# Optimization experiments

Measured on AMD Instinct MI355X. Metric: run time of the kernel, lower is better.

Reference implementation:

```python
import jax, jax.numpy as jnp
import numpy as np

V, B, T, C, H, L = 32000, 4, 1024, 1024, 16, 8
HS = C // H  # head_size = 64


def _ln(x, g, b):
    m = x.mean(-1, keepdims=True)
    v = x.var(-1, keepdims=True)
    return (x - m) / jnp.sqrt(v + 1e-5) * g + b


def setup_inputs() -> dict:
    key = jax.random.key(0)
    ks = jax.random.split(key, 24)
    s = 0.02
    inp = {
        "idx": jax.random.randint(ks[0], (B, T), 0, V, dtype=jnp.int64),
        "tok_emb": jax.random.normal(ks[1], (V, C), jnp.float32) * s,
        "pos_emb": jax.random.normal(ks[2], (T, C), jnp.float32) * s,
        "Wq": jax.random.normal(ks[3], (L, H, C, HS), jnp.float32) * s,
        "Wk": jax.random.normal(ks[4], (L, H, C, HS), jnp.float32) * s,
        "Wv": jax.random.normal(ks[5], (L, H, C, HS), jnp.float32) * s,
        "Ph_w": jax.random.normal(ks[6], (L, H, HS, C), jnp.float32) * s,
        "Ph_b": jnp.zeros((L, H, C), jnp.float32),
        "Pm_w": jax.random.normal(ks[7], (L, C, C), jnp.float32) * s,
        "Pm_b": jnp.zeros((L, C), jnp.float32),
        "ln1_g": jnp.ones((L, C), jnp.float32),
        "ln1_b": jnp.zeros((L, C), jnp.float32),
        "ln2_g": jnp.ones((L, C), jnp.float32),
        "ln2_b": jnp.zeros((L, C), jnp.float32),
        "W1": jax.random.normal(ks[8], (L, C, 4 * C), jnp.float32) * s,
        "b1": jnp.zeros((L, 4 * C), jnp.float32),
        "W2": jax.random.normal(ks[9], (L, 4 * C, C), jnp.float32) * s,
        "b2": jnp.zeros((L, C), jnp.float32),
        "lnf_g": jnp.ones((C,), jnp.float32),
        "lnf_b": jnp.zeros((C,), jnp.float32),
        "head_w": jax.random.normal(ks[10], (C, V), jnp.float32) * s,
        "head_b": jnp.zeros((V,), jnp.float32),
    }
    return inp


def reference(idx, tok_emb, pos_emb, Wq, Wk, Wv, Ph_w, Ph_b, Pm_w, Pm_b,
              ln1_g, ln1_b, ln2_g, ln2_b, W1, b1, W2, b2, lnf_g, lnf_b,
              head_w, head_b):
    Bx, Tx = idx.shape
    x = tok_emb[idx] + pos_emb[:Tx]  # [B,T,C]
    mask = jnp.tril(jnp.ones((Tx, Tx), bool))
    scale = x.shape[-1] ** -0.5  # NOTE: original scales by n_embd**-0.5, not head_size
    n_layers = Wq.shape[0]
    for l in range(n_layers):
        xn = _ln(x, ln1_g[l], ln1_b[l])
        q = jnp.einsum('btc,hcs->bhts', xn, Wq[l])
        k = jnp.einsum('btc,hcs->bhts', xn, Wk[l])
        v = jnp.einsum('btc,hcs->bhts', xn, Wv[l])
        wei = jnp.einsum('bhts,bhus->bhtu', q, k) * scale
        wei = jnp.where(mask, wei, -jnp.inf)
        wei = jax.nn.softmax(wei, axis=-1)
        o = jnp.einsum('bhtu,bhus->bhts', wei, v)  # [B,H,T,HS]
        per = jnp.einsum('bhts,hsc->bhtc', o, Ph_w[l]) + Ph_b[l][None, :, None, :]
        sa = per.sum(axis=1) @ Pm_w[l] + Pm_b[l]  # combine heads, final proj
        x = x + sa
        xn2 = _ln(x, ln2_g[l], ln2_b[l])
        h = jax.nn.gelu(xn2 @ W1[l] + b1[l], approximate=False)
        x = x + h @ W2[l] + b2[l]
    x = _ln(x, lnf_g, lnf_b)
    return x @ head_w + head_b  # logits [B,T,V]
```

## Files before the change

### kernel.cpp

```cpp
#include <hip/hip_runtime.h>
#include <hip/hip_bf16.h>
#include <math.h>

static constexpr int V = 32000, B = 4, T = 1024, C = 1024, H = 16, NL = 8, HS = 64;
static constexpr int M = B * T;

typedef __bf16 bf16x8 __attribute__((ext_vector_type(8)));
typedef __bf16 bf16x4 __attribute__((ext_vector_type(4)));
typedef float f32x4 __attribute__((ext_vector_type(4)));

#define AS1 __attribute__((address_space(1)))
#define AS3 __attribute__((address_space(3)))

__global__ void k_embed(const int* __restrict__ idx, const float* __restrict__ tok,
                        const float* __restrict__ pos, float* __restrict__ x) {
  int g = blockIdx.x * blockDim.x + threadIdx.x;
  if (g >= M * C / 4) return;
  int c4 = g & 255;
  int bt = g >> 8;
  int t = bt & (T - 1);
  int row = idx[bt];
  float4 tv = *(const float4*)(tok + (size_t)row * C + c4 * 4);
  float4 pv = *(const float4*)(pos + (size_t)t * C + c4 * 4);
  float4 o;
  o.x = tv.x + pv.x; o.y = tv.y + pv.y; o.z = tv.z + pv.z; o.w = tv.w + pv.w;
  *(float4*)(x + (size_t)bt * C + c4 * 4) = o;
}

__global__ __launch_bounds__(256) void k_ln_bf(const float* __restrict__ x, const float* __restrict__ g,
                                               const float* __restrict__ b, __hip_bfloat16* __restrict__ y) {
  int row = blockIdx.x, tid = threadIdx.x;
  float4 v = ((const float4*)(x + (size_t)row * C))[tid];
  float s = v.x + v.y + v.z + v.w;
  float ss = v.x * v.x + v.y * v.y + v.z * v.z + v.w * v.w;
  for (int off = 32; off > 0; off >>= 1) {
    s += __shfl_down(s, off);
    ss += __shfl_down(ss, off);
  }
  __shared__ float sb[4], qb[4];
  int wid = tid >> 6;
  if ((tid & 63) == 0) { sb[wid] = s; qb[wid] = ss; }
  __syncthreads();
  float st = sb[0] + sb[1] + sb[2] + sb[3];
  float qt = qb[0] + qb[1] + qb[2] + qb[3];
  float mean = st * (1.0f / C);
  float var = qt * (1.0f / C) - mean * mean;
  float rstd = rsqrtf(var + 1e-5f);
  float4 gv = ((const float4*)g)[tid];
  float4 bv = ((const float4*)b)[tid];
  union { __hip_bfloat16 h[4]; ushort4 u; } pk;
  pk.h[0] = __float2bfloat16((v.x - mean) * rstd * gv.x + bv.x);
  pk.h[1] = __float2bfloat16((v.y - mean) * rstd * gv.y + bv.y);
  pk.h[2] = __float2bfloat16((v.z - mean) * rstd * gv.z + bv.z);
  pk.h[3] = __float2bfloat16((v.w - mean) * rstd * gv.w + bv.w);
  *(ushort4*)(y + (size_t)row * C + tid * 4) = pk.u;
}

__device__ __forceinline__ void transp_block(const float* __restrict__ in, __hip_bfloat16* __restrict__ out,
                                             int K, int N, int bx, int by, float (*t)[65]) {
  int n0 = bx * 64, k0 = by * 64;
  int tx = threadIdx.x & 15, ty = threadIdx.x >> 4;
#pragma unroll
  for (int i = 0; i < 64; i += 16) {
    float4 v = *(const float4*)(in + (size_t)(k0 + ty + i) * N + n0 + tx * 4);
    t[ty + i][tx * 4 + 0] = v.x;
    t[ty + i][tx * 4 + 1] = v.y;
    t[ty + i][tx * 4 + 2] = v.z;
    t[ty + i][tx * 4 + 3] = v.w;
  }
  __syncthreads();
#pragma unroll
  for (int i = 0; i < 64; i += 16) {
    int n = ty + i;
    union { __hip_bfloat16 h[4]; ushort4 u; } pk;
#pragma unroll
    for (int j = 0; j < 4; ++j) pk.h[j] = __float2bfloat16(t[tx * 4 + j][n]);
    *(ushort4*)(out + (size_t)(n0 + n) * K + k0 + tx * 4) = pk.u;
  }
}

__global__ __launch_bounds__(256) void k_transp(const float* __restrict__ in, __hip_bfloat16* __restrict__ out,
                                                int K, int N) {
  __shared__ float t[64][65];
  transp_block(in, out, K, N, blockIdx.x, blockIdx.y, t);
}

__global__ __launch_bounds__(256) void k_prep(const float* __restrict__ Wq, const float* __restrict__ Wk,
                                              const float* __restrict__ Wv, const float* __restrict__ Pm,
                                              const float* __restrict__ Ph, const float* __restrict__ W1,
                                              const float* __restrict__ W2,
                                              __hip_bfloat16* __restrict__ qkvw, __hip_bfloat16* __restrict__ pmT,
                                              __hip_bfloat16* __restrict__ phB, __hip_bfloat16* __restrict__ w1T,
                                              __hip_bfloat16* __restrict__ w2T) {
  __shared__ float tls[64][65];
  int bid = blockIdx.x;
  if (bid < 768) {
    int bx = bid & 15, z = bid >> 4;
    int sel = z >> 4, h = z & 15;
    const float* W = sel == 0 ? Wq : (sel == 1 ? Wk : Wv);
    const float* in = W + (size_t)h * C * HS;
    __hip_bfloat16* o = qkvw + ((size_t)sel * 1024 + h * 64) * C;
    int k0 = bx * 64;
    int tx = threadIdx.x & 15, ty = threadIdx.x >> 4;
#pragma unroll
    for (int i = 0; i < 64; i += 16) {
      float4 v = *(const float4*)(in + (size_t)(k0 + ty + i) * HS + tx * 4);
      tls[ty + i][tx * 4 + 0] = v.x;
      tls[ty + i][tx * 4 + 1] = v.y;
      tls[ty + i][tx * 4 + 2] = v.z;
      tls[ty + i][tx * 4 + 3] = v.w;
    }
    __syncthreads();
#pragma unroll
    for (int i = 0; i < 64; i += 16) {
      int n = ty + i;
      union { __hip_bfloat16 h4[4]; ushort4 u; } pk;
#pragma unroll
      for (int j = 0; j < 4; ++j) pk.h4[j] = __float2bfloat16(tls[tx * 4 + j][n]);
      *(ushort4*)(o + (size_t)n * C + k0 + tx * 4) = pk.u;
    }
  } else if (bid < 1024) {
    int r = bid - 768;
    transp_block(Pm, pmT, C, C, r & 15, r >> 4, tls);
  } else if (bid < 2048) {
    int g = (bid - 1024) * 256 + threadIdx.x;
    float4 v = ((const float4*)Ph)[g];
    union { __hip_bfloat16 h[4]; ushort4 u; } pk;
    pk.h[0] = __float2bfloat16(v.x);
    pk.h[1] = __float2bfloat16(v.y);
    pk.h[2] = __float2bfloat16(v.z);
    pk.h[3] = __float2bfloat16(v.w);
    ((ushort4*)phB)[g] = pk.u;
  } else if (bid < 3072) {
    int r = bid - 2048;
    transp_block(W1, w1T, C, 4 * C, r & 63, r >> 6, tls);
  } else {
    int r = bid - 3072;
    transp_block(W2, w2T, 4 * C, C, r & 15, r >> 4, tls);
  }
}

__global__ __launch_bounds__(256) void k_biasc(const float* __restrict__ phb, const float* __restrict__ Pm,
                                               const float* __restrict__ Pmb, float* __restrict__ bc) {
  __shared__ float bs[1024];
  __shared__ float red[4][64];
  int tid = threadIdx.x;
#pragma unroll
  for (int q = 0; q < 4; ++q) {
    int c = tid * 4 + q;
    float s = 0.0f;
    for (int h = 0; h < H; ++h) s += phb[(size_t)h * C + c];
    bs[c] = s;
  }
  __syncthreads();
  int c = blockIdx.x * 64 + (tid & 63);
  int part = tid >> 6;
  float s = 0.0f;
  for (int j = part * 256; j < part * 256 + 256; ++j) s += bs[j] * Pm[(size_t)j * C + c];
  red[part][tid & 63] = s;
  __syncthreads();
  if (tid < 64)
    bc[blockIdx.x * 64 + tid] = Pmb[blockIdx.x * 64 + tid] + red[0][tid] + red[1][tid] + red[2][tid] + red[3][tid];
}

template <int BIAS, int GELU, int RES, int OUTBF>
__global__ __launch_bounds__(256) void k_gemm_bf(const __hip_bfloat16* __restrict__ A,
                                                 const __hip_bfloat16* __restrict__ Bt,
                                                 void* Cout, const float* __restrict__ bias,
                                                 const float* res, int N, int K) {
  __shared__ __align__(16) __hip_bfloat16 As[128 * 32];
  __shared__ __align__(16) __hip_bfloat16 Bs[128 * 32];
  int bm = blockIdx.y * 128, bn = blockIdx.x * 128;
  int tid = threadIdx.x;
  int w = tid >> 6, l = tid & 63;
  int wr = (w >> 1) * 64, wc = (w & 1) * 64;
  int lr = l >> 2;
  int lk = (l & 3) * 8;
  int fr = l & 15;
  int fk = (l >> 4) * 8;
  const __hip_bfloat16* Ag = A + (size_t)bm * K;
  const __hip_bfloat16* Bg = Bt + (size_t)bn * K;
  f32x4 acc[4][4];
#pragma unroll
  for (int m = 0; m < 4; ++m)
#pragma unroll
    for (int n = 0; n < 4; ++n) acc[m][n] = (f32x4){0.f, 0.f, 0.f, 0.f};

  for (int k0 = 0; k0 < K; k0 += 32) {
    __syncthreads();
#pragma unroll
    for (int i = 0; i < 2; ++i) {
      int seg = w * 2 + i;
      int r = seg * 16 + lr;
      __builtin_amdgcn_global_load_lds((const AS1 void*)(Ag + (size_t)r * K + k0 + lk),
                                       (AS3 void*)(As + seg * 512), 16, 0, 0);
      __builtin_amdgcn_global_load_lds((const AS1 void*)(Bg + (size_t)r * K + k0 + lk),
                                       (AS3 void*)(Bs + seg * 512), 16, 0, 0);
    }
    __syncthreads();
    bf16x8 af[4], bfr[4];
#pragma unroll
    for (int m = 0; m < 4; ++m) af[m] = *(const bf16x8*)(As + ((size_t)(wr + m * 16 + fr)) * 32 + fk);
#pragma unroll
    for (int n = 0; n < 4; ++n) bfr[n] = *(const bf16x8*)(Bs + ((size_t)(wc + n * 16 + fr)) * 32 + fk);
#pragma unroll
    for (int m = 0; m < 4; ++m)
#pragma unroll
      for (int n = 0; n < 4; ++n)
        acc[m][n] = __builtin_amdgcn_mfma_f32_16x16x32_bf16(af[m], bfr[n], acc[m][n], 0, 0, 0);
  }
  int crow0 = (l >> 4) * 4;
  int ccol = l & 15;
#pragma unroll
  for (int m = 0; m < 4; ++m) {
    int row = bm + wr + m * 16 + crow0;
#pragma unroll
    for (int n = 0; n < 4; ++n) {
      int col = bn + wc + n * 16 + ccol;
      float bv = BIAS ? bias[col] : 0.0f;
#pragma unroll
      for (int r = 0; r < 4; ++r) {
        float v = acc[m][n][r] + bv;
        if (GELU) v = 0.5f * v * (1.0f + erff(v * 0.70710678118f));
        if (RES) v += res[(size_t)(row + r) * N + col];
        if (OUTBF)
          ((__hip_bfloat16*)Cout)[(size_t)(row + r) * N + col] = __float2bfloat16(v);
        else
          ((float*)Cout)[(size_t)(row + r) * N + col] = v;
      }
    }
  }
}

template <int BIAS, int GELU, int RES, int OUTBF>
__global__ __launch_bounds__(512, 2) void k_gemm256(const __hip_bfloat16* __restrict__ Ah,
                                                    const __hip_bfloat16* __restrict__ Bth,
                                                    void* Cout, const float* __restrict__ bias,
                                                    const float* res, int N, int K) {
  __shared__ __align__(16) __bf16 As[4][256 * 32];
  __shared__ __align__(16) __bf16 Bs[4][256 * 32];
  const __bf16* A = (const __bf16*)Ah;
  const __bf16* Bt = (const __bf16*)Bth;
  const int nx = N >> 8;
  const int bid = blockIdx.x;
  const int sw = ((bid & 7) * ((int)gridDim.x >> 3)) + (bid >> 3);
  const int bn = (sw % nx) << 8;
  const int bm = (sw / nx) << 8;
  const int tid = threadIdx.x, w = tid >> 6, l = tid & 63;
  const int wm = w >> 2, wn = w & 3;
  const int fr = l & 15, fg = l >> 4;
  const int srow = w * 32 + (l >> 2);
  const int scole = ((((l & 3) << 4) ^ ((l & 8) << 2) ^ (l & 16)) >> 1);
  const __bf16* Ag = A + (size_t)(bm + srow) * K + scole;
  const __bf16* Bg = Bt + (size_t)(bn + srow) * K + scole;
  const int arow = wm * 128 + fr;
  const int brow = wn * 64 + fr;
  const int koff = (((fg * 16) ^ (((fr & 2) << 4) | ((fr & 4) << 2))) >> 1);

  f32x4 acc[8][4];
#pragma unroll
  for (int m = 0; m < 8; ++m)
#pragma unroll
    for (int n = 0; n < 4; ++n) acc[m][n] = (f32x4){0.f, 0.f, 0.f, 0.f};

  auto stage = [&](int bufi, int tt) {
    size_t kb = (size_t)tt * 32;
#pragma unroll
    for (int jj = 0; jj < 2; ++jj) {
      __builtin_amdgcn_global_load_lds((const AS1 void*)(Ag + (size_t)jj * 16 * K + kb),
                                       (AS3 void*)(&As[bufi][(w * 32 + jj * 16) * 32]), 16, 0, 0);
      __builtin_amdgcn_global_load_lds((const AS1 void*)(Bg + (size_t)jj * 16 * K + kb),
                                       (AS3 void*)(&Bs[bufi][(w * 32 + jj * 16) * 32]), 16, 0, 0);
    }
  };

  bf16x8 fa[2][8], fb[2][4];

#define READF(SET, BI)                                                              \
  {                                                                                 \
    const int bi_ = (BI);                                                           \
    _Pragma("unroll") for (int mg = 0; mg < 8; ++mg)                                \
        fa[SET][mg] = *(const bf16x8*)(&As[bi_][(arow + mg * 16) * 32 + koff]);     \
    _Pragma("unroll") for (int ng = 0; ng < 4; ++ng)                                \
        fb[SET][ng] = *(const bf16x8*)(&Bs[bi_][(brow + ng * 16) * 32 + koff]);     \
  }

#define MFMAS(SET)                                                                  \
  _Pragma("unroll") for (int mg = 0; mg < 8; ++mg)                                  \
      _Pragma("unroll") for (int ng = 0; ng < 4; ++ng)                              \
          acc[mg][ng] =                                                             \
              __builtin_amdgcn_mfma_f32_16x16x32_bf16(fa[SET][mg], fb[SET][ng], acc[mg][ng], 0, 0, 0);

#define GITER(T, CUR, NXT)                                                          \
  {                                                                                 \
    const int t_ = (T);                                                             \
    asm volatile("s_waitcnt lgkmcnt(0)" ::: "memory");                              \
    if (t_ + 2 < NT)                                                                \
      asm volatile("s_waitcnt vmcnt(4)" ::: "memory");                              \
    else                                                                            \
      asm volatile("s_waitcnt vmcnt(0)" ::: "memory");                              \
    __builtin_amdgcn_sched_barrier(0);                                              \
    __builtin_amdgcn_s_barrier();                                                   \
    __builtin_amdgcn_sched_barrier(0);                                              \
    if (t_ + 1 < NT) READF(NXT, (t_ + 1) & 3);                                      \
    if (t_ + 3 < NT) stage((t_ + 3) & 3, t_ + 3);                                   \
    __builtin_amdgcn_s_setprio(1);                                                  \
    MFMAS(CUR);                                                                     \
    __builtin_amdgcn_s_setprio(0);                                                  \
  }

  const int NT = K >> 5;
  stage(0, 0);
  stage(1, 1);
  stage(2, 2);
  asm volatile("s_waitcnt vmcnt(8)" ::: "memory");
  __builtin_amdgcn_sched_barrier(0);
  __builtin_amdgcn_s_barrier();
  __builtin_amdgcn_sched_barrier(0);
  READF(0, 0);

  for (int t = 0; t < NT; t += 2) {
    GITER(t, 0, 1);
    GITER(t + 1, 1, 0);
  }
#undef READF
#undef MFMAS
#undef GITER

#pragma unroll
  for (int mg = 0; mg < 8; ++mg) {
    int row = bm + wm * 128 + mg * 16 + fg * 4;
#pragma unroll
    for (int n = 0; n < 4; ++n) {
      int col = bn + wn * 64 + n * 16 + fr;
      float bvx = BIAS ? bias[col] : 0.0f;
#pragma unroll
      for (int r = 0; r < 4; ++r) {
        float v = acc[mg][n][r] + bvx;
        if (GELU) v = 0.5f * v * (1.0f + erff(v * 0.70710678118f));
        if (RES) v += res[(size_t)(row + r) * N + col];
        if (OUTBF)
          ((__hip_bfloat16*)Cout)[(size_t)(row + r) * N + col] = __float2bfloat16(v);
        else
          ((float*)Cout)[(size_t)(row + r) * N + col] = v;
      }
    }
  }
}

__global__ __launch_bounds__(256) void k_attn(const __hip_bfloat16* __restrict__ qkvh,
                                              __hip_bfloat16* __restrict__ o) {
  const __bf16* qkv = (const __bf16*)qkvh;
  int qi = blockIdx.x;
  int bh = blockIdx.y;
  int b = bh >> 4, h = bh & 15;
  int tid = threadIdx.x;
  int w = tid >> 6, l = tid & 63;
  int fr = l & 15, fg = l >> 4;
  int qw = qi * 64 + w * 16;

  __shared__ __align__(16) __bf16 Ks[32][72];
  __shared__ __align__(16) __bf16 Vt[64][40];
  __shared__ __align__(16) __bf16 Ps[4][16][40];

  const size_t bT = (size_t)b * T;
  bf16x8 a_q[2];
  {
    const __bf16* qp = qkv + (bT + qw + fr) * 3072 + h * 64 + fg * 8;
    a_q[0] = *(const bf16x8*)qp;
    a_q[1] = *(const bf16x8*)(qp + 32);
  }
  f32x4 acc_o[4];
#pragma unroll
  for (int n = 0; n < 4; ++n) acc_o[n] = (f32x4){0.f, 0.f, 0.f, 0.f};
  float mrow[4] = {-1e30f, -1e30f, -1e30f, -1e30f};
  float lrow[4] = {0.f, 0.f, 0.f, 0.f};

  int sr = tid >> 3;
  int sc = (tid & 7) * 8;
  int ntile = (qi + 1) * 2;
  for (int t = 0; t < ntile; ++t) {
    int kv0 = t * 32;
    __syncthreads();
    {
      const __bf16* kp = qkv + (bT + kv0 + sr) * 3072 + 1024 + h * 64 + sc;
      bf16x8 k8 = *(const bf16x8*)kp;
      bf16x8 v8 = *(const bf16x8*)(kp + 1024);
      *(bf16x8*)&Ks[sr][sc] = k8;
#pragma unroll
      for (int j = 0; j < 8; ++j) Vt[sc + j][sr] = v8[j];
    }
    __syncthreads();
    if (kv0 > qw + 15) continue;

    f32x4 s0 = (f32x4){0.f, 0.f, 0.f, 0.f}, s1 = s0;
    s0 = __builtin_amdgcn_mfma_f32_16x16x32_bf16(a_q[0], *(const bf16x8*)&Ks[fr][fg * 8], s0, 0, 0, 0);
    s0 = __builtin_amdgcn_mfma_f32_16x16x32_bf16(a_q[1], *(const bf16x8*)&Ks[fr][32 + fg * 8], s0, 0, 0, 0);
    s1 = __builtin_amdgcn_mfma_f32_16x16x32_bf16(a_q[0], *(const bf16x8*)&Ks[16 + fr][fg * 8], s1, 0, 0, 0);
    s1 = __builtin_amdgcn_mfma_f32_16x16x32_bf16(a_q[1], *(const bf16x8*)&Ks[16 + fr][32 + fg * 8], s1, 0, 0, 0);

    int qrow = qw + fg * 4;
#pragma unroll
    for (int r = 0; r < 4; ++r) { s0[r] *= 0.03125f; s1[r] *= 0.03125f; }
    if (kv0 + 31 > qw) {
#pragma unroll
      for (int r = 0; r < 4; ++r) {
        if (kv0 + fr > qrow + r) s0[r] = -1e30f;
        if (kv0 + 16 + fr > qrow + r) s1[r] = -1e30f;
      }
    }
    float tm[4], psum[4], alpha[4];
#pragma unroll
    for (int r = 0; r < 4; ++r) tm[r] = fmaxf(s0[r], s1[r]);
#pragma unroll
    for (int off = 1; off < 16; off <<= 1)
#pragma unroll
      for (int r = 0; r < 4; ++r) tm[r] = fmaxf(tm[r], __shfl_xor(tm[r], off));
#pragma unroll
    for (int r = 0; r < 4; ++r) {
      float mnew = fmaxf(mrow[r], tm[r]);
      alpha[r] = __expf(mrow[r] - mnew);
      mrow[r] = mnew;
      float p0 = __expf(s0[r] - mnew);
      float p1 = __expf(s1[r] - mnew);
      s0[r] = p0; s1[r] = p1;
      psum[r] = p0 + p1;
    }
#pragma unroll
    for (int off = 1; off < 16; off <<= 1)
#pragma unroll
      for (int r = 0; r < 4; ++r) psum[r] += __shfl_xor(psum[r], off);
#pragma unroll
    for (int r = 0; r < 4; ++r) lrow[r] = lrow[r] * alpha[r] + psum[r];
#pragma unroll
    for (int n = 0; n < 4; ++n)
#pragma unroll
      for (int r = 0; r < 4; ++r) acc_o[n][r] *= alpha[r];

#pragma unroll
    for (int r = 0; r < 4; ++r) {
      Ps[w][fg * 4 + r][fr] = (__bf16)s0[r];
      Ps[w][fg * 4 + r][16 + fr] = (__bf16)s1[r];
    }
    bf16x8 a_p = *(const bf16x8*)&Ps[w][fr][fg * 8];
#pragma unroll
    for (int n = 0; n < 4; ++n) {
      bf16x8 bvv = *(const bf16x8*)&Vt[n * 16 + fr][fg * 8];
      acc_o[n] = __builtin_amdgcn_mfma_f32_16x16x32_bf16(a_p, bvv, acc_o[n], 0, 0, 0);
    }
  }
  float inv[4];
#pragma unroll
  for (int r = 0; r < 4; ++r) inv[r] = 1.0f / lrow[r];
  __bf16* ob = (__bf16*)o;
#pragma unroll
  for (int n = 0; n < 4; ++n)
#pragma unroll
    for (int r = 0; r < 4; ++r)
      ob[(bT + qw + fg * 4 + r) * 1024 + h * 64 + n * 16 + fr] = (__bf16)(acc_o[n][r] * inv[r]);
}

extern "C" void kernel_launch(void* const* d_in, const int* in_sizes, int n_in,
                              void* d_out, int out_size, void* d_ws, size_t ws_size,
                              hipStream_t stream) {
  const int* idx = (const int*)d_in[0];
  const float* tok = (const float*)d_in[1];
  const float* pos = (const float*)d_in[2];
  const float* Wq = (const float*)d_in[3];
  const float* Wk = (const float*)d_in[4];
  const float* Wv = (const float*)d_in[5];
  const float* Phw = (const float*)d_in[6];
  const float* Phb = (const float*)d_in[7];
  const float* Pmw = (const float*)d_in[8];
  const float* Pmb = (const float*)d_in[9];
  const float* ln1g = (const float*)d_in[10];
  const float* ln1b = (const float*)d_in[11];
  const float* ln2g = (const float*)d_in[12];
  const float* ln2b = (const float*)d_in[13];
  const float* W1 = (const float*)d_in[14];
  const float* b1 = (const float*)d_in[15];
  const float* W2 = (const float*)d_in[16];
  const float* b2 = (const float*)d_in[17];
  const float* lnfg = (const float*)d_in[18];
  const float* lnfb = (const float*)d_in[19];
  const float* headw = (const float*)d_in[20];
  const float* headb = (const float*)d_in[21];
  float* out = (float*)d_out;

  char* p = (char*)d_ws;
  float* x = (float*)p;                        p += (size_t)M * C * 4;
  float* bcv = (float*)p;                      p += 4096;
  char* layer_region = p;
  __hip_bfloat16* qkvb = (__hip_bfloat16*)p;   p += (size_t)M * 3072 * 2;
  __hip_bfloat16* ob = (__hip_bfloat16*)p;     p += (size_t)M * C * 2;
  __hip_bfloat16* hb = (__hip_bfloat16*)p;     p += (size_t)M * 4 * C * 2;
  __hip_bfloat16* xn = (__hip_bfloat16*)p;     p += (size_t)M * C * 2;
  __hip_bfloat16* qkvw = (__hip_bfloat16*)p;   p += (size_t)3 * C * C * 2;
  __hip_bfloat16* pmT = (__hip_bfloat16*)p;    p += (size_t)C * C * 2;
  __hip_bfloat16* phB = (__hip_bfloat16*)p;    p += (size_t)C * C * 2;
  __hip_bfloat16* wcombT = (__hip_bfloat16*)p; p += (size_t)C * C * 2;
  __hip_bfloat16* w1T = (__hip_bfloat16*)p;    p += (size_t)4 * C * C * 2;
  __hip_bfloat16* w2T = (__hip_bfloat16*)p;    p += (size_t)4 * C * C * 2;
  __hip_bfloat16* wt_head = (__hip_bfloat16*)layer_region;

  k_embed<<<(M * C / 4 + 255) / 256, 256, 0, stream>>>(idx, tok, pos, x);

  for (int l = 0; l < NL; ++l) {
    k_ln_bf<<<M, 256, 0, stream>>>(x, ln1g + (size_t)l * C, ln1b + (size_t)l * C, xn);
    k_prep<<<4096, 256, 0, stream>>>(Wq + (size_t)l * H * C * HS, Wk + (size_t)l * H * C * HS,
                                     Wv + (size_t)l * H * C * HS, Pmw + (size_t)l * C * C,
                                     Phw + (size_t)l * H * HS * C, W1 + (size_t)l * C * 4 * C,
                                     W2 + (size_t)l * 4 * C * C, qkvw, pmT, phB, w1T, w2T);
    k_gemm256<0, 0, 0, 1><<<(3072 / 256) * (M / 256), 512, 0, stream>>>(xn, qkvw, qkvb, nullptr, nullptr, 3072, C);
    k_attn<<<dim3(T / 64, B * H), 256, 0, stream>>>(qkvb, ob);
    k_biasc<<<16, 256, 0, stream>>>(Phb + (size_t)l * H * C, Pmw + (size_t)l * C * C, Pmb + (size_t)l * C, bcv);
    k_gemm_bf<0, 0, 0, 1><<<dim3(C / 128, C / 128), 256, 0, stream>>>(pmT, phB, wcombT, nullptr, nullptr, C, C);
    k_gemm_bf<1, 0, 1, 0><<<dim3(C / 128, M / 128), 256, 0, stream>>>(ob, wcombT, x, bcv, x, C, C);
    k_ln_bf<<<M, 256, 0, stream>>>(x, ln2g + (size_t)l * C, ln2b + (size_t)l * C, xn);
    k_gemm256<1, 1, 0, 1><<<(4 * C / 256) * (M / 256), 512, 0, stream>>>(xn, w1T, hb, b1 + (size_t)l * 4 * C, nullptr, 4 * C, C);
    k_gemm_bf<1, 0, 1, 0><<<dim3(C / 128, M / 128), 256, 0, stream>>>(hb, w2T, x, b2 + (size_t)l * C, x, C, 4 * C);
  }

  k_ln_bf<<<M, 256, 0, stream>>>(x, lnfg, lnfb, xn);
  k_transp<<<dim3(500, 16), 256, 0, stream>>>(headw, wt_head, C, V);
  k_gemm256<1, 0, 0, 0><<<(V / 256) * (M / 256), 512, 0, stream>>>(xn, wt_head, out, headb, nullptr, V, C);
}
```

Baseline: 3.717 ms.

## Double-buffer K/V tiles in attention, reverse query-block order, drop V transpose

The attention kernel now prefetches the next K/V tile into registers while computing on the current one, and keeps two shared-memory buffers so global loads overlap the MFMA and softmax work. V is stored row-major with a padded stride instead of being transposed on store, and the MFMA operand is gathered with strided LDS reads. Query blocks are launched in reverse order so the longest causal blocks start first, which should improve load balance. The costs are more LDS use per block, extra registers for the prefetch, and eight scalar LDS reads per V operand.

Result: faster. 3.622 ms (-2.6%).

```diff
diff --git a/kernel.cpp b/kernel.cpp
--- a/kernel.cpp
+++ b/kernel.cpp
@@ -351,7 +351,7 @@
 __global__ __launch_bounds__(256) void k_attn(const __hip_bfloat16* __restrict__ qkvh,
                                               __hip_bfloat16* __restrict__ o) {
   const __bf16* qkv = (const __bf16*)qkvh;
-  int qi = blockIdx.x;
+  int qi = (int)gridDim.x - 1 - (int)blockIdx.x;
   int bh = blockIdx.y;
   int b = bh >> 4, h = bh & 15;
   int tid = threadIdx.x;
@@ -359,8 +359,8 @@
   int fr = l & 15, fg = l >> 4;
   int qw = qi * 64 + w * 16;
 
-  __shared__ __align__(16) __bf16 Ks[32][72];
-  __shared__ __align__(16) __bf16 Vt[64][40];
+  __shared__ __align__(16) __bf16 Ks[2][32][72];
+  __shared__ __align__(16) __bf16 Vs[2][32][76];
   __shared__ __align__(16) __bf16 Ps[4][16][40];
 
   const size_t bT = (size_t)b * T;
@@ -379,75 +379,92 @@
   int sr = tid >> 3;
   int sc = (tid & 7) * 8;
   int ntile = (qi + 1) * 2;
+  const __bf16* kbase = qkv + (bT + sr) * 3072 + 1024 + h * 64 + sc;
+
+  {
+    bf16x8 k8 = *(const bf16x8*)kbase;
+    bf16x8 v8 = *(const bf16x8*)(kbase + 1024);
+    *(bf16x8*)&Ks[0][sr][sc] = k8;
+    *(bf16x4*)&Vs[0][sr][sc] = __builtin_shufflevector(v8, v8, 0, 1, 2, 3);
+    *(bf16x4*)&Vs[0][sr][sc + 4] = __builtin_shufflevector(v8, v8, 4, 5, 6, 7);
+  }
+  __syncthreads();
+
   for (int t = 0; t < ntile; ++t) {
     int kv0 = t * 32;
+    int cur = t & 1;
+    bf16x8 k8n, v8n;
+    if (t + 1 < ntile) {
+      const __bf16* kp = kbase + (size_t)(t + 1) * 32 * 3072;
+      k8n = *(const bf16x8*)kp;
+      v8n = *(const bf16x8*)(kp + 1024);
+    }
+    if (kv0 <= qw + 15) {
+      f32x4 s0 = (f32x4){0.f, 0.f, 0.f, 0.f}, s1 = s0;
+      s0 = __builtin_amdgcn_mfma_f32_16x16x32_bf16(a_q[0], *(const bf16x8*)&Ks[cur][fr][fg * 8], s0, 0, 0, 0);
+      s0 = __builtin_amdgcn_mfma_f32_16x16x32_bf16(a_q[1], *(const bf16x8*)&Ks[cur][fr][32 + fg * 8], s0, 0, 0, 0);
+      s1 = __builtin_amdgcn_mfma_f32_16x16x32_bf16(a_q[0], *(const bf16x8*)&Ks[cur][16 + fr][fg * 8], s1, 0, 0, 0);
+      s1 = __builtin_amdgcn_mfma_f32_16x16x32_bf16(a_q[1], *(const bf16x8*)&Ks[cur][16 + fr][32 + fg * 8], s1, 0, 0, 0);
+
+      int qrow = qw + fg * 4;
+#pragma unroll
+      for (int r = 0; r < 4; ++r) { s0[r] *= 0.03125f; s1[r] *= 0.03125f; }
+      if (kv0 + 31 > qw) {
+#pragma unroll
+        for (int r = 0; r < 4; ++r) {
+          if (kv0 + fr > qrow + r) s0[r] = -1e30f;
+          if (kv0 + 16 + fr > qrow + r) s1[r] = -1e30f;
+        }
+      }
+      float tm[4], psum[4], alpha[4];
+#pragma unroll
+      for (int r = 0; r < 4; ++r) tm[r] = fmaxf(s0[r], s1[r]);
+#pragma unroll
+      for (int off = 1; off < 16; off <<= 1)
+#pragma unroll
+        for (int r = 0; r < 4; ++r) tm[r] = fmaxf(tm[r], __shfl_xor(tm[r], off));
+#pragma unroll
+      for (int r = 0; r < 4; ++r) {
+        float mnew = fmaxf(mrow[r], tm[r]);
+        alpha[r] = __expf(mrow[r] - mnew);
+        mrow[r] = mnew;
+        float p0 = __expf(s0[r] - mnew);
+        float p1 = __expf(s1[r] - mnew);
+        s0[r] = p0; s1[r] = p1;
+        psum[r] = p0 + p1;
+      }
+#pragma unroll
+      for (int off = 1; off < 16; off <<= 1)
+#pragma unroll
+        for (int r = 0; r < 4; ++r) psum[r] += __shfl_xor(psum[r], off);
+#pragma unroll
+      for (int r = 0; r < 4; ++r) lrow[r] = lrow[r] * alpha[r] + psum[r];
+#pragma unroll
+      for (int n = 0; n < 4; ++n)
+#pragma unroll
+        for (int r = 0; r < 4; ++r) acc_o[n][r] *= alpha[r];
+
+#pragma unroll
+      for (int r = 0; r < 4; ++r) {
+        Ps[w][fg * 4 + r][fr] = (__bf16)s0[r];
+        Ps[w][fg * 4 + r][16 + fr] = (__bf16)s1[r];
+      }
+      bf16x8 a_p = *(const bf16x8*)&Ps[w][fr][fg * 8];
+#pragma unroll
+      for (int n = 0; n < 4; ++n) {
+        bf16x8 bvv;
+#pragma unroll
+        for (int j = 0; j < 8; ++j) bvv[j] = Vs[cur][fg * 8 + j][n * 16 + fr];
+        acc_o[n] = __builtin_amdgcn_mfma_f32_16x16x32_bf16(a_p, bvv, acc_o[n], 0, 0, 0);
+      }
+    }
     __syncthreads();
-    {
-      const __bf16* kp = qkv + (bT + kv0 + sr) * 3072 + 1024 + h * 64 + sc;
-      bf16x8 k8 = *(const bf16x8*)kp;
-      bf16x8 v8 = *(const bf16x8*)(kp + 1024);
-      *(bf16x8*)&Ks[sr][sc] = k8;
-#pragma unroll
-      for (int j = 0; j < 8; ++j) Vt[sc + j][sr] = v8[j];
+    if (t + 1 < ntile) {
+      *(bf16x8*)&Ks[cur ^ 1][sr][sc] = k8n;
+      *(bf16x4*)&Vs[cur ^ 1][sr][sc] = __builtin_shufflevector(v8n, v8n, 0, 1, 2, 3);
+      *(bf16x4*)&Vs[cur ^ 1][sr][sc + 4] = __builtin_shufflevector(v8n, v8n, 4, 5, 6, 7);
     }
     __syncthreads();
-    if (kv0 > qw + 15) continue;
-
-    f32x4 s0 = (f32x4){0.f, 0.f, 0.f, 0.f}, s1 = s0;
-    s0 = __builtin_amdgcn_mfma_f32_16x16x32_bf16(a_q[0], *(const bf16x8*)&Ks[fr][fg * 8], s0, 0, 0, 0);
-    s0 = __builtin_amdgcn_mfma_f32_16x16x32_bf16(a_q[1], *(const bf16x8*)&Ks[fr][32 + fg * 8], s0, 0, 0, 0);
-    s1 = __builtin_amdgcn_mfma_f32_16x16x32_bf16(a_q[0], *(const bf16x8*)&Ks[16 + fr][fg * 8], s1, 0, 0, 0);
-    s1 = __builtin_amdgcn_mfma_f32_16x16x32_bf16(a_q[1], *(const bf16x8*)&Ks[16 + fr][32 + fg * 8], s1, 0, 0, 0);
-
-    int qrow = qw + fg * 4;
-#pragma unroll
-    for (int r = 0; r < 4; ++r) { s0[r] *= 0.03125f; s1[r] *= 0.03125f; }
-    if (kv0 + 31 > qw) {
-#pragma unroll
-      for (int r = 0; r < 4; ++r) {
-        if (kv0 + fr > qrow + r) s0[r] = -1e30f;
-        if (kv0 + 16 + fr > qrow + r) s1[r] = -1e30f;
-      }
-    }
-    float tm[4], psum[4], alpha[4];
-#pragma unroll
-    for (int r = 0; r < 4; ++r) tm[r] = fmaxf(s0[r], s1[r]);
-#pragma unroll
-    for (int off = 1; off < 16; off <<= 1)
-#pragma unroll
-      for (int r = 0; r < 4; ++r) tm[r] = fmaxf(tm[r], __shfl_xor(tm[r], off));
-#pragma unroll
-    for (int r = 0; r < 4; ++r) {
-      float mnew = fmaxf(mrow[r], tm[r]);
-      alpha[r] = __expf(mrow[r] - mnew);
-      mrow[r] = mnew;
-      float p0 = __expf(s0[r] - mnew);
-      float p1 = __expf(s1[r] - mnew);
-      s0[r] = p0; s1[r] = p1;
-      psum[r] = p0 + p1;
-    }
-#pragma unroll
-    for (int off = 1; off < 16; off <<= 1)
-#pragma unroll
-      for (int r = 0; r < 4; ++r) psum[r] += __shfl_xor(psum[r], off);
-#pragma unroll
-    for (int r = 0; r < 4; ++r) lrow[r] = lrow[r] * alpha[r] + psum[r];
-#pragma unroll
-    for (int n = 0; n < 4; ++n)
-#pragma unroll
-      for (int r = 0; r < 4; ++r) acc_o[n][r] *= alpha[r];
-
-#pragma unroll
-    for (int r = 0; r < 4; ++r) {
-      Ps[w][fg * 4 + r][fr] = (__bf16)s0[r];
-      Ps[w][fg * 4 + r][16 + fr] = (__bf16)s1[r];
-    }
-    bf16x8 a_p = *(const bf16x8*)&Ps[w][fr][fg * 8];
-#pragma unroll
-    for (int n = 0; n < 4; ++n) {
-      bf16x8 bvv = *(const bf16x8*)&Vt[n * 16 + fr][fg * 8];
-      acc_o[n] = __builtin_amdgcn_mfma_f32_16x16x32_bf16(a_p, bvv, acc_o[n], 0, 0, 0);
-    }
   }
   float inv[4];
 #pragma unroll
```
